# Optimization experiments

Hardware: AMD Instinct MI355X
Metric: run time of the kernel (lower is better)

Reference implementation:

```python
import jax, jax.numpy as jnp
import numpy as np

HEADS = 8
DIM_HEAD = 64
ROPE_THETA = 10000.0


def _rope(t):
    # t: [b, h, n, d]; interleaved-pair rotation as in rotary-embedding-torch
    n, d = t.shape[-2], t.shape[-1]
    inv_freq = 1.0 / (ROPE_THETA ** (jnp.arange(0, d, 2, dtype=jnp.float32) / d))  # [d/2]
    freqs = jnp.arange(n, dtype=jnp.float32)[:, None] * inv_freq[None, :]  # [n, d/2]
    freqs = jnp.repeat(freqs, 2, axis=-1)  # [n, d], repeated per pair
    cos, sin = jnp.cos(freqs), jnp.sin(freqs)
    x1 = t[..., 0::2]
    x2 = t[..., 1::2]
    rot = jnp.stack((-x2, x1), axis=-1).reshape(t.shape)  # rotate_half
    return t * cos + rot * sin


def setup_inputs() -> dict:
    key = jax.random.key(0)
    k1, k2, k3, k4 = jax.random.split(key, 4)
    b, n, dim = 2, 2048, 512
    hidden = HEADS * DIM_HEAD
    x = jax.random.normal(k1, (b, n, dim), dtype=jnp.float32)
    pos_bias = jax.random.normal(k2, (HEADS, n, n), dtype=jnp.float32) * 0.02
    w_qkv = jax.random.normal(k3, (dim, 3 * hidden), dtype=jnp.float32) * (dim ** -0.5)
    w_out = jax.random.normal(k4, (hidden, dim), dtype=jnp.float32) * (hidden ** -0.5)
    return {"x": x, "pos_bias": pos_bias, "w_qkv": w_qkv, "w_out": w_out}


def reference(x, pos_bias, w_qkv, w_out):
    b, n, _ = x.shape
    qkv = x @ w_qkv  # [b, n, 3*hidden]
    q, k, v = jnp.split(qkv, 3, axis=-1)

    def to_heads(t):
        return t.reshape(b, n, HEADS, DIM_HEAD).transpose(0, 2, 1, 3)  # [b,h,n,d]

    q, k, v = map(to_heads, (q, k, v))
    k = _rope(k)
    q = _rope(q * (DIM_HEAD ** -0.5))
    sim = jnp.einsum('bhid,bhjd->bhij', q, k)  # [b,h,n,n]
    sim = sim + pos_bias  # broadcast over batch
    sim = sim - jax.lax.stop_gradient(jnp.max(sim, axis=-1, keepdims=True))
    attn = jax.nn.softmax(sim, axis=-1)
    out = jnp.einsum('bhij,bhjd->bhid', attn, v)
    out = out.transpose(0, 2, 1, 3).reshape(b, n, HEADS * DIM_HEAD)
    return out @ w_out
```

## Files before the change

kernel.cpp:

```cpp
#include <hip/hip_runtime.h>
#include <math.h>

#define SEQ 2048
#define NHEAD 8
#define HDIM 64
#define BATCH 2

typedef __attribute__((ext_vector_type(8))) short short8;
typedef __attribute__((ext_vector_type(4))) float f32x4;

__device__ __forceinline__ ushort f2bf(float f) {
    union { float f; unsigned u; } v; v.f = f;
    unsigned r = v.u + 0x7FFFu + ((v.u >> 16) & 1u);
    return (ushort)(r >> 16);
}

__device__ __forceinline__ f32x4 mfma16(short8 a, short8 b, f32x4 c) {
    return __builtin_amdgcn_mfma_f32_16x16x32_bf16(a, b, c, 0, 0, 0);
}

__device__ __forceinline__ void gld16(const void* g, void* l) {
    __builtin_amdgcn_global_load_lds(
        (const __attribute__((address_space(1))) unsigned int*)g,
        (__attribute__((address_space(3))) unsigned int*)l, 16, 0, 0);
}

__global__ __launch_bounds__(256)
void prep(const float* __restrict__ x, const float* __restrict__ w_qkv,
          const float* __restrict__ w_out, ushort* __restrict__ xb,
          ushort* __restrict__ wqkvT, ushort* __restrict__ woutT)
{
    __shared__ ushort tile[64][66];
    const int blk = blockIdx.x, t = threadIdx.x;
    if (blk < 1024) {
        const int i = (blk * 256 + t) * 8;
        float4 a = *(const float4*)&x[i];
        float4 b = *(const float4*)&x[i + 4];
        union { ushort us[8]; uint4 v; } pk;
        pk.us[0] = f2bf(a.x); pk.us[1] = f2bf(a.y); pk.us[2] = f2bf(a.z); pk.us[3] = f2bf(a.w);
        pk.us[4] = f2bf(b.x); pk.us[5] = f2bf(b.y); pk.us[6] = f2bf(b.z); pk.us[7] = f2bf(b.w);
        *(uint4*)&xb[i] = pk.v;
        return;
    }
    const float* w; ushort* wT; int K, N, n0, k0;
    if (blk < 1216) { const int s = blk - 1024; w = w_qkv; wT = wqkvT; K = 512; N = 1536; n0 = (s % 24) * 64; k0 = (s / 24) * 64; }
    else            { const int s = blk - 1216; w = w_out; wT = woutT; K = 512; N = 512;  n0 = (s % 8) * 64;  k0 = (s / 8) * 64; }
#pragma unroll
    for (int i = 0; i < 4; ++i) {
        const int slot = t + i * 256;
        const int r = slot >> 4, c4 = (slot & 15) * 4;
        float4 v = *(const float4*)&w[(size_t)(k0 + r) * N + n0 + c4];
        tile[c4 + 0][r] = f2bf(v.x);
        tile[c4 + 1][r] = f2bf(v.y);
        tile[c4 + 2][r] = f2bf(v.z);
        tile[c4 + 3][r] = f2bf(v.w);
    }
    __syncthreads();
    const int n = t >> 2, kc = (t & 3) * 16;
    union { ushort us[16]; uint4 v[2]; } o;
#pragma unroll
    for (int j = 0; j < 16; ++j) o.us[j] = tile[n][kc + j];
    *(uint4*)&wT[(size_t)(n0 + n) * K + k0 + kc]     = o.v[0];
    *(uint4*)&wT[(size_t)(n0 + n) * K + k0 + kc + 8] = o.v[1];
}

__global__ __launch_bounds__(256)
void gemm_qkv_rope(const ushort* __restrict__ xb, const ushort* __restrict__ wT,
                   ushort* __restrict__ qb, ushort* __restrict__ kb,
                   ushort* __restrict__ vtb)
{
    __shared__ __align__(16) ushort As[64][64];
    __shared__ __align__(16) ushort Bs[128][64];
    const int t = threadIdx.x, lane = t & 63, w = t >> 6;
    const int quad = lane >> 4, l16 = lane & 15;
    const int m0 = blockIdx.y * 64, n0 = blockIdx.x * 128;
    const int mw = (w >> 1) * 32, nw = (w & 1) * 64;
    const int krow = lane >> 3, kcol = (lane & 7) * 8;
    f32x4 acc[2][4] = {};

    for (int k0 = 0; k0 < 512; k0 += 64) {
        __syncthreads();
        gld16(&xb[(size_t)(m0 + w * 8 + krow) * 512 + k0 + kcol],        &As[w * 8][0]);
        gld16(&xb[(size_t)(m0 + (w + 4) * 8 + krow) * 512 + k0 + kcol],  &As[(w + 4) * 8][0]);
#pragma unroll
        for (int jj = 0; jj < 4; ++jj) {
            const int j = w * 4 + jj;
            gld16(&wT[(size_t)(n0 + j * 8 + krow) * 512 + k0 + kcol], &Bs[j * 8][0]);
        }
        __syncthreads();
#pragma unroll
        for (int ks = 0; ks < 2; ++ks) {
            short8 a[2], b[4];
#pragma unroll
            for (int i = 0; i < 2; ++i)
                a[i] = *(const short8*)&As[mw + i * 16 + l16][ks * 32 + quad * 8];
#pragma unroll
            for (int j = 0; j < 4; ++j)
                b[j] = *(const short8*)&Bs[nw + j * 16 + l16][ks * 32 + quad * 8];
#pragma unroll
            for (int i = 0; i < 2; ++i)
#pragma unroll
                for (int j = 0; j < 4; ++j)
                    acc[i][j] = mfma16(a[i], b[j], acc[i][j]);
        }
    }

    const int sec = (n0 + nw) >> 9;
    if (sec == 2) {
#pragma unroll
        for (int i = 0; i < 2; ++i) {
            const int m = m0 + mw + i * 16 + quad * 4;
            const int bidx = m >> 11, n = m & 2047;
#pragma unroll
            for (int j = 0; j < 4; ++j) {
                const int nc = n0 + nw + j * 16 + l16;
                const int d = nc & 63, h = (nc >> 6) & 7;
                ushort4 pk;
                pk.x = f2bf(acc[i][j][0]); pk.y = f2bf(acc[i][j][1]);
                pk.z = f2bf(acc[i][j][2]); pk.w = f2bf(acc[i][j][3]);
                *(ushort4*)&vtb[(((size_t)bidx * 8 + h) * 64 + d) * 2048 + n] = pk;
            }
        }
    } else {
        ushort* dst = (sec == 0) ? qb : kb;
        const float scale = (sec == 0) ? 0.125f : 1.0f;
#pragma unroll
        for (int j = 0; j < 4; ++j) {
            const int nc = n0 + nw + j * 16 + l16;
            const int d = nc & 63, h = (nc >> 6) & 7;
            const float inv = __expf(-(float)(d & ~1) * (9.2103403719761836f / 64.0f));
#pragma unroll
            for (int i = 0; i < 2; ++i)
#pragma unroll
            for (int r = 0; r < 4; ++r) {
                const int m = m0 + mw + i * 16 + quad * 4 + r;
                const int bidx = m >> 11, n = m & 2047;
                float sn, cs;
                __sincosf((float)n * inv, &sn, &cs);
                const float vacc = acc[i][j][r];
                const float partner = __shfl_xor(vacc, 1);
                const float rot = (d & 1) ? (vacc * cs + partner * sn)
                                          : (vacc * cs - partner * sn);
                dst[(((size_t)bidx * 8 + h) * 2048 + n) * 64 + d] = f2bf(rot * scale);
            }
        }
    }
}

__global__ __launch_bounds__(256)
void flash_attn_mfma(const ushort* __restrict__ qb, const ushort* __restrict__ kb,
                     const ushort* __restrict__ vtb, const float* __restrict__ bias,
                     ushort* __restrict__ ob)
{
    __shared__ __align__(16) ushort Ks[2][64][64];
    __shared__ __align__(16) ushort Vt[2][64][64];
    __shared__ __align__(16) float  Bl[2][64][64];
    __shared__ __align__(16) ushort Ps[4][16][72];
    const int t = threadIdx.x, lane = t & 63, w = t >> 6;
    const int quad = lane >> 4, l16 = lane & 15;
    const int q0 = blockIdx.x * 64, h = blockIdx.y, b = blockIdx.z;
    const size_t bh = (size_t)(b * NHEAD + h);
    const ushort* Q  = qb  + bh * SEQ * HDIM;
    const ushort* Kp = kb  + bh * SEQ * HDIM;
    const ushort* VT = vtb + bh * HDIM * SEQ;

    short8 qf[2];
    qf[0] = *(const short8*)&Q[(size_t)(q0 + w * 16 + l16) * HDIM + quad * 8];
    qf[1] = *(const short8*)&Q[(size_t)(q0 + w * 16 + l16) * HDIM + 32 + quad * 8];

    f32x4 oacc[4] = {};
    float lsum[4] = {};
    const int krow = lane >> 3;
    const int kcolsw = ((lane & 7) ^ krow) * 8;
    const int brow = lane >> 4, bcol = (lane & 15) * 4;

    const int sw = l16 & 7;
    const int c0 = (quad ^ sw) * 8;
    const int c1 = ((quad + 4) ^ sw) * 8;

    auto stage = [&](int buf, int it_) {
        const int k0 = it_ * 64;
        gld16(&Kp[(size_t)(k0 + w * 8 + krow) * HDIM + kcolsw],       &Ks[buf][w * 8][0]);
        gld16(&Kp[(size_t)(k0 + (w + 4) * 8 + krow) * HDIM + kcolsw], &Ks[buf][(w + 4) * 8][0]);
        gld16(&VT[(size_t)(w * 8 + krow) * SEQ + k0 + kcolsw],        &Vt[buf][w * 8][0]);
        gld16(&VT[(size_t)((w + 4) * 8 + krow) * SEQ + k0 + kcolsw],  &Vt[buf][(w + 4) * 8][0]);
#pragma unroll
        for (int jj = 0; jj < 4; ++jj) {
            const int j = w * 4 + jj;
            gld16(&bias[((size_t)h * SEQ + q0 + j * 4 + brow) * SEQ + k0 + bcol], &Bl[buf][j * 4][0]);
        }
    };

    stage(0, 0);
    __syncthreads();

    for (int it = 0; it < 32; ++it) {
        const int cur = it & 1;
        if (it + 1 < 32) stage(cur ^ 1, it + 1);

        f32x4 sacc[4] = {};
#pragma unroll
        for (int s = 0; s < 4; ++s) {
            short8 kf0 = *(const short8*)&Ks[cur][s * 16 + l16][c0];
            sacc[s] = mfma16(qf[0], kf0, sacc[s]);
            short8 kf1 = *(const short8*)&Ks[cur][s * 16 + l16][c1];
            sacc[s] = mfma16(qf[1], kf1, sacc[s]);
        }

#pragma unroll
        for (int r = 0; r < 4; ++r)
#pragma unroll
            for (int s = 0; s < 4; ++s) {
                const float p = __expf(sacc[s][r] + Bl[cur][w * 16 + quad * 4 + r][s * 16 + l16]);
                lsum[r] += p;
                Ps[w][quad * 4 + r][s * 16 + l16] = f2bf(p);
            }
        asm volatile("" ::: "memory");

#pragma unroll
        for (int ks = 0; ks < 2; ++ks) {
            short8 pf = *(const short8*)&Ps[w][l16][ks * 32 + quad * 8];
            const int cc = ks ? c1 : c0;
#pragma unroll
            for (int s = 0; s < 4; ++s) {
                short8 vf = *(const short8*)&Vt[cur][s * 16 + l16][cc];
                oacc[s] = mfma16(pf, vf, oacc[s]);
            }
        }

        __syncthreads();
    }

#pragma unroll
    for (int r = 0; r < 4; ++r) {
        float rs = lsum[r];
        rs += __shfl_xor(rs, 1, 16);
        rs += __shfl_xor(rs, 2, 16);
        rs += __shfl_xor(rs, 4, 16);
        rs += __shfl_xor(rs, 8, 16);
        const float invl = 1.0f / rs;
        const size_t m = (size_t)b * SEQ + q0 + w * 16 + quad * 4 + r;
#pragma unroll
        for (int s = 0; s < 4; ++s)
            ob[m * 512 + h * HDIM + s * 16 + l16] = f2bf(oacc[s][r] * invl);
    }
}

__global__ __launch_bounds__(256)
void gemm_out(const ushort* __restrict__ Ab, const ushort* __restrict__ wT,
              float* __restrict__ C)
{
    __shared__ __align__(16) ushort As[64][64];
    __shared__ __align__(16) ushort Bs[64][64];
    const int t = threadIdx.x, lane = t & 63, w = t >> 6;
    const int quad = lane >> 4, l16 = lane & 15;
    const int m0 = blockIdx.y * 64, n0 = blockIdx.x * 64;
    const int mw = (w >> 1) * 32, nw = (w & 1) * 32;
    const int krow = lane >> 3, kcol = (lane & 7) * 8;
    f32x4 acc[2][2] = {};

    for (int k0 = 0; k0 < 512; k0 += 64) {
        __syncthreads();
        gld16(&Ab[(size_t)(m0 + w * 8 + krow) * 512 + k0 + kcol],       &As[w * 8][0]);
        gld16(&Ab[(size_t)(m0 + (w + 4) * 8 + krow) * 512 + k0 + kcol], &As[(w + 4) * 8][0]);
        gld16(&wT[(size_t)(n0 + w * 8 + krow) * 512 + k0 + kcol],       &Bs[w * 8][0]);
        gld16(&wT[(size_t)(n0 + (w + 4) * 8 + krow) * 512 + k0 + kcol], &Bs[(w + 4) * 8][0]);
        __syncthreads();
#pragma unroll
        for (int ks = 0; ks < 2; ++ks) {
            short8 a[2], b[2];
#pragma unroll
            for (int i = 0; i < 2; ++i)
                a[i] = *(const short8*)&As[mw + i * 16 + l16][ks * 32 + quad * 8];
#pragma unroll
            for (int j = 0; j < 2; ++j)
                b[j] = *(const short8*)&Bs[nw + j * 16 + l16][ks * 32 + quad * 8];
#pragma unroll
            for (int i = 0; i < 2; ++i)
#pragma unroll
                for (int j = 0; j < 2; ++j)
                    acc[i][j] = mfma16(a[i], b[j], acc[i][j]);
        }
    }
#pragma unroll
    for (int i = 0; i < 2; ++i)
#pragma unroll
    for (int r = 0; r < 4; ++r) {
        const int m = m0 + mw + i * 16 + quad * 4 + r;
#pragma unroll
        for (int j = 0; j < 2; ++j)
            C[(size_t)m * 512 + n0 + nw + j * 16 + l16] = acc[i][j][r];
    }
}

extern "C" void kernel_launch(void* const* d_in, const int* in_sizes, int n_in,
                              void* d_out, int out_size, void* d_ws, size_t ws_size,
                              hipStream_t stream)
{
    const float* x        = (const float*)d_in[0];
    const float* pos_bias = (const float*)d_in[1];
    const float* w_qkv    = (const float*)d_in[2];
    const float* w_out    = (const float*)d_in[3];
    float* out = (float*)d_out;

    char* ws = (char*)d_ws;
    ushort* xb     = (ushort*)(ws);
    ushort* wqkvT  = (ushort*)(ws + 4194304);
    ushort* woutT  = (ushort*)(ws + 5767168);
    ushort* qb     = (ushort*)(ws + 6291456);
    ushort* kb     = (ushort*)(ws + 10485760);
    ushort* vtb    = (ushort*)(ws + 14680064);
    ushort* attnb  = (ushort*)(ws + 18874368);

    prep<<<1280, 256, 0, stream>>>(x, w_qkv, w_out, xb, wqkvT, woutT);
    gemm_qkv_rope<<<dim3(12, 64), 256, 0, stream>>>(xb, wqkvT, qb, kb, vtb);
    flash_attn_mfma<<<dim3(SEQ / 64, NHEAD, BATCH), 256, 0, stream>>>(qb, kb, vtb, pos_bias, attnb);
    gemm_out<<<dim3(8, 64), 256, 0, stream>>>(attnb, woutT, out);
}
```

Baseline: 257.4 us.

## Triple-buffer K/V in LDS and load position bias directly into registers

The attention kernel no longer stages the position-bias tile through LDS. Each lane now loads its 16 bias values straight into registers, two iterations ahead, using two alternating register sets. K/V staging moves to a three-buffer LDS ring with manual vmcnt waits and raw barriers in place of __syncthreads, and s_setprio boosts priority around the MFMA sections. This aims to cut LDS traffic and footprint and hide global latency better. In exchange it uses more registers and depends on hand-counted vmcnt values, which break if the number of in-flight loads changes.

```diff
diff --git a/kernel.cpp b/kernel.cpp
--- a/kernel.cpp
+++ b/kernel.cpp
@@ -152,9 +152,8 @@
                      const ushort* __restrict__ vtb, const float* __restrict__ bias,
                      ushort* __restrict__ ob)
 {
-    __shared__ __align__(16) ushort Ks[2][64][64];
-    __shared__ __align__(16) ushort Vt[2][64][64];
-    __shared__ __align__(16) float  Bl[2][64][64];
+    __shared__ __align__(16) ushort Ks[3][64][64];
+    __shared__ __align__(16) ushort Vt[3][64][64];
     __shared__ __align__(16) ushort Ps[4][16][72];
     const int t = threadIdx.x, lane = t & 63, w = t >> 6;
     const int quad = lane >> 4, l16 = lane & 15;
@@ -163,73 +162,104 @@
     const ushort* Q  = qb  + bh * SEQ * HDIM;
     const ushort* Kp = kb  + bh * SEQ * HDIM;
     const ushort* VT = vtb + bh * HDIM * SEQ;
-
-    short8 qf[2];
-    qf[0] = *(const short8*)&Q[(size_t)(q0 + w * 16 + l16) * HDIM + quad * 8];
-    qf[1] = *(const short8*)&Q[(size_t)(q0 + w * 16 + l16) * HDIM + 32 + quad * 8];
+    const float*  Bp = bias + ((size_t)h * SEQ + q0 + w * 16) * SEQ;
 
     f32x4 oacc[4] = {};
     float lsum[4] = {};
     const int krow = lane >> 3;
     const int kcolsw = ((lane & 7) ^ krow) * 8;
-    const int brow = lane >> 4, bcol = (lane & 15) * 4;
 
     const int sw = l16 & 7;
     const int c0 = (quad ^ sw) * 8;
     const int c1 = ((quad + 4) ^ sw) * 8;
 
-    auto stage = [&](int buf, int it_) {
-        const int k0 = it_ * 64;
-        gld16(&Kp[(size_t)(k0 + w * 8 + krow) * HDIM + kcolsw],       &Ks[buf][w * 8][0]);
-        gld16(&Kp[(size_t)(k0 + (w + 4) * 8 + krow) * HDIM + kcolsw], &Ks[buf][(w + 4) * 8][0]);
-        gld16(&VT[(size_t)(w * 8 + krow) * SEQ + k0 + kcolsw],        &Vt[buf][w * 8][0]);
-        gld16(&VT[(size_t)((w + 4) * 8 + krow) * SEQ + k0 + kcolsw],  &Vt[buf][(w + 4) * 8][0]);
-#pragma unroll
-        for (int jj = 0; jj < 4; ++jj) {
-            const int j = w * 4 + jj;
-            gld16(&bias[((size_t)h * SEQ + q0 + j * 4 + brow) * SEQ + k0 + bcol], &Bl[buf][j * 4][0]);
-        }
-    };
-
-    stage(0, 0);
-    __syncthreads();
-
-    for (int it = 0; it < 32; ++it) {
-        const int cur = it & 1;
-        if (it + 1 < 32) stage(cur ^ 1, it + 1);
-
-        f32x4 sacc[4] = {};
-#pragma unroll
-        for (int s = 0; s < 4; ++s) {
-            short8 kf0 = *(const short8*)&Ks[cur][s * 16 + l16][c0];
-            sacc[s] = mfma16(qf[0], kf0, sacc[s]);
-            short8 kf1 = *(const short8*)&Ks[cur][s * 16 + l16][c1];
-            sacc[s] = mfma16(qf[1], kf1, sacc[s]);
-        }
-
-#pragma unroll
-        for (int r = 0; r < 4; ++r)
-#pragma unroll
-            for (int s = 0; s < 4; ++s) {
-                const float p = __expf(sacc[s][r] + Bl[cur][w * 16 + quad * 4 + r][s * 16 + l16]);
-                lsum[r] += p;
-                Ps[w][quad * 4 + r][s * 16 + l16] = f2bf(p);
-            }
-        asm volatile("" ::: "memory");
-
-#pragma unroll
-        for (int ks = 0; ks < 2; ++ks) {
-            short8 pf = *(const short8*)&Ps[w][l16][ks * 32 + quad * 8];
-            const int cc = ks ? c1 : c0;
-#pragma unroll
-            for (int s = 0; s < 4; ++s) {
-                short8 vf = *(const short8*)&Vt[cur][s * 16 + l16][cc];
-                oacc[s] = mfma16(pf, vf, oacc[s]);
-            }
-        }
-
-        __syncthreads();
-    }
+    short8 qf[2];
+    qf[0] = *(const short8*)&Q[(size_t)(q0 + w * 16 + l16) * HDIM + quad * 8];
+    qf[1] = *(const short8*)&Q[(size_t)(q0 + w * 16 + l16) * HDIM + 32 + quad * 8];
+    asm volatile("" ::: "memory");
+
+    float b0[16], b1[16];
+
+#define FA_STAGE(BUF, IT_)                                                          \
+    {                                                                               \
+        const int k2_ = (IT_) * 64;                                                 \
+        gld16(&Kp[(size_t)(k2_ + w * 8 + krow) * HDIM + kcolsw],       &Ks[BUF][w * 8][0]);       \
+        gld16(&Kp[(size_t)(k2_ + (w + 4) * 8 + krow) * HDIM + kcolsw], &Ks[BUF][(w + 4) * 8][0]); \
+        gld16(&VT[(size_t)(w * 8 + krow) * SEQ + k2_ + kcolsw],        &Vt[BUF][w * 8][0]);       \
+        gld16(&VT[(size_t)((w + 4) * 8 + krow) * SEQ + k2_ + kcolsw],  &Vt[BUF][(w + 4) * 8][0]); \
+    }
+
+#define FA_BIAS(BREG, IT_)                                                          \
+    {                                                                               \
+        const int k2_ = (IT_) * 64;                                                 \
+        _Pragma("unroll")                                                           \
+        for (int r = 0; r < 4; ++r)                                                 \
+            _Pragma("unroll")                                                       \
+            for (int s = 0; s < 4; ++s)                                             \
+                BREG[r * 4 + s] = Bp[(size_t)(quad * 4 + r) * SEQ + k2_ + s * 16 + l16]; \
+    }
+
+#define FA_BODY(IT, BCUR, REFILL, WCNT)                                             \
+    {                                                                               \
+        asm volatile("s_waitcnt vmcnt(" #WCNT ")" ::: "memory");                    \
+        __builtin_amdgcn_s_barrier();                                               \
+        const int cb_ = (IT) % 3;                                                   \
+        if (REFILL) {                                                               \
+            FA_STAGE(((IT) + 2) % 3, (IT) + 2);                                     \
+            asm volatile("" ::: "memory");              \
+        }                                                                           \
+        f32x4 sacc[4] = {};                                                         \
+        __builtin_amdgcn_s_setprio(1);                                              \
+        _Pragma("unroll")                                                           \
+        for (int s = 0; s < 4; ++s) {                                               \
+            short8 kf0 = *(const short8*)&Ks[cb_][s * 16 + l16][c0];                \
+            sacc[s] = mfma16(qf[0], kf0, sacc[s]);                                  \
+            short8 kf1 = *(const short8*)&Ks[cb_][s * 16 + l16][c1];                \
+            sacc[s] = mfma16(qf[1], kf1, sacc[s]);                                  \
+        }                                                                           \
+        __builtin_amdgcn_s_setprio(0);                                              \
+        _Pragma("unroll")                                                           \
+        for (int r = 0; r < 4; ++r)                                                 \
+            _Pragma("unroll")                                                       \
+            for (int s = 0; s < 4; ++s) {                                           \
+                const float p = __expf(sacc[s][r] + BCUR[r * 4 + s]);               \
+                lsum[r] += p;                                                       \
+                Ps[w][quad * 4 + r][s * 16 + l16] = f2bf(p);                        \
+            }                                                                       \
+        if (REFILL) FA_BIAS(BCUR, (IT) + 2);                                        \
+        asm volatile("" ::: "memory");               \
+        __builtin_amdgcn_s_setprio(1);                                              \
+        _Pragma("unroll")                                                           \
+        for (int ks = 0; ks < 2; ++ks) {                                            \
+            short8 pf = *(const short8*)&Ps[w][l16][ks * 32 + quad * 8];            \
+            const int cc_ = ks ? c1 : c0;                                           \
+            _Pragma("unroll")                                                       \
+            for (int s = 0; s < 4; ++s) {                                           \
+                short8 vf = *(const short8*)&Vt[cb_][s * 16 + l16][cc_];            \
+                oacc[s] = mfma16(pf, vf, oacc[s]);                                  \
+            }                                                                       \
+        }                                                                           \
+        __builtin_amdgcn_s_setprio(0);                                              \
+    }
+
+    FA_STAGE(0, 0);
+    asm volatile("" ::: "memory");
+    FA_BIAS(b0, 0);
+    asm volatile("" ::: "memory");
+    FA_STAGE(1, 1);
+    asm volatile("" ::: "memory");
+    FA_BIAS(b1, 1);
+
+    for (int i2 = 0; i2 < 15; ++i2) {
+        FA_BODY(2 * i2,     b0, 1, 36);
+        FA_BODY(2 * i2 + 1, b1, 1, 36);
+    }
+    FA_BODY(30, b0, 0, 36);
+    FA_BODY(31, b1, 0, 16);
+
+#undef FA_BODY
+#undef FA_BIAS
+#undef FA_STAGE
 
 #pragma unroll
     for (int r = 0; r < 4; ++r) {
```

New measurement: 251.1 us. -2.4%, faster.
